# Optimization experiments

Measured on AMD Instinct MI355X. Metric: run time of the kernel, lower is better.

## Reference

```python
import jax, jax.numpy as jnp
import numpy as np

B, T, IN, H, K = 128, 4096, 2, 64, 2  # batch, seq_len, input feat, lstm hidden, num tags


def setup_inputs() -> dict:
    key = jax.random.key(0)
    ks = jax.random.split(key, 16)
    s = 1.0 / np.sqrt(H)
    u = lambda k, shape, a: jax.random.uniform(k, shape, jnp.float32, -a, a)
    p = {}
    p['x'] = jax.random.normal(ks[0], (B, T, IN), jnp.float32)
    # layer 0 (input IN), layer 1 (input 2H); leading dim 2 = [forward, backward] direction
    p['w_ih0'] = u(ks[1], (2, 4 * H, IN), s)
    p['w_hh0'] = u(ks[2], (2, 4 * H, H), s)
    p['b_ih0'] = u(ks[3], (2, 4 * H), s)
    p['b_hh0'] = u(ks[4], (2, 4 * H), s)
    p['w_ih1'] = u(ks[5], (2, 4 * H, 2 * H), s)
    p['w_hh1'] = u(ks[6], (2, 4 * H, H), s)
    p['b_ih1'] = u(ks[7], (2, 4 * H), s)
    p['b_hh1'] = u(ks[8], (2, 4 * H), s)
    p['fc_w'] = u(ks[9], (K, 2 * H), 1.0 / np.sqrt(2 * H))
    p['fc_b'] = u(ks[10], (K,), 1.0 / np.sqrt(2 * H))
    # CRF params (torchcrf init: U(-0.1, 0.1))
    p['trans'] = u(ks[11], (K, K), 0.1)
    p['start'] = u(ks[12], (K,), 0.1)
    p['end'] = u(ks[13], (K,), 0.1)
    return p


def _lstm_dir(xg, w_hh, b_hh):
    # xg: [T, B, 4H] precomputed input projections; PyTorch gate order i, f, g, o
    b, h = xg.shape[1], w_hh.shape[1]

    def step(carry, g_x):
        hs, cs = carry
        g = g_x + hs @ w_hh.T + b_hh
        i, f, gg, o = jnp.split(g, 4, axis=-1)
        cs = jax.nn.sigmoid(f) * cs + jax.nn.sigmoid(i) * jnp.tanh(gg)
        hs = jax.nn.sigmoid(o) * jnp.tanh(cs)
        return (hs, cs), hs

    init = (jnp.zeros((b, h), xg.dtype), jnp.zeros((b, h), xg.dtype))
    _, out = jax.lax.scan(step, init, xg)
    return out  # [T, B, H]


def _bilstm_layer(xt, w_ih, w_hh, b_ih, b_hh):
    # xt: [T, B, F] time-major input
    xg_f = jnp.einsum('tbi,gi->tbg', xt, w_ih[0]) + b_ih[0]
    xg_b = jnp.einsum('tbi,gi->tbg', xt[::-1], w_ih[1]) + b_ih[1]
    hf = _lstm_dir(xg_f, w_hh[0], b_hh[0])
    hb = _lstm_dir(xg_b, w_hh[1], b_hh[1])[::-1]
    return jnp.concatenate([hf, hb], axis=-1)  # [T, B, 2H]


def _viterbi(logits, trans, start, end):
    # logits: [B, T, K] -> best path [B, T]
    e = jnp.swapaxes(logits, 0, 1)  # [T, B, K]
    score0 = start[None, :] + e[0]

    def fwd(score, e_t):
        cand = score[:, :, None] + trans[None, :, :]  # [B, Kprev, Knext]
        bp = jnp.argmax(cand, axis=1)
        return jnp.max(cand, axis=1) + e_t, bp

    score, bps = jax.lax.scan(fwd, score0, e[1:])  # bps: [T-1, B, K]
    last = jnp.argmax(score + end[None, :], axis=-1)  # [B]

    def back(tag, bp):
        prev = jnp.take_along_axis(bp, tag[:, None], axis=1)[:, 0]
        return prev, prev

    _, path = jax.lax.scan(back, last, bps, reverse=True)  # [T-1, B]
    return jnp.swapaxes(jnp.concatenate([path, last[None, :]], axis=0), 0, 1)


def reference(x, w_ih0, w_hh0, b_ih0, b_hh0, w_ih1, w_hh1, b_ih1, b_hh1,
              fc_w, fc_b, trans, start, end):
    xt = jnp.swapaxes(x, 0, 1)  # [T, B, IN]
    h0 = _bilstm_layer(xt, w_ih0, w_hh0, b_ih0, b_hh0)
    h1 = _bilstm_layer(h0, w_ih1, w_hh1, b_ih1, b_hh1)  # [T, B, 2H]
    logits = jnp.swapaxes(jnp.einsum('tbh,kh->tbk', h1, fc_w) + fc_b, 0, 1)  # [B, T, K]
    return _viterbi(logits, trans, start, end).astype(jnp.int32)
```

## Files before the change

### kernel.cpp

```cpp
#include <hip/hip_runtime.h>

#define TT 4096
#define BATCH 128
#define HID 64
#define CK 32
#define NCH (TT / CK)
#define NSLOT (NCH + 1)

__device__ __forceinline__ float sigm(float x) { return 1.f / (1.f + expf(-x)); }
__device__ __forceinline__ float tanh_f(float x) { float e = expf(2.f * x); return 1.f - 2.f / (e + 1.f); }

__global__ __launch_bounds__(512, 2) void lstm_ckpt(
    const float* __restrict__ x,
    const float* __restrict__ w_ih,
    const float* __restrict__ w_hh,
    const float* __restrict__ b_ih, const float* __restrict__ b_hh,
    float* __restrict__ ckpt)
{
    const int blk = blockIdx.x;
    const int dir = blk & 1;
    const int b   = blk >> 1;
    const int tid = threadIdx.x;
    const int row = tid >> 1, half = tid & 1;

    __shared__ __align__(16) float xs[TT * 2];
    __shared__ __align__(16) float h_lds[HID];
    __shared__ __align__(16) float g_lds[256];

    {
        const float4* src = (const float4*)(x + (size_t)b * TT * 2);
        float4* dst = (float4*)xs;
        for (int rr = tid; rr < 2048; rr += 512) dst[rr] = src[rr];
    }
    const int grow = dir * 256 + row;
    float wv[32];
    {
        const float4* wr = (const float4*)(w_hh + (size_t)grow * 64) + half * 8;
        #pragma unroll
        for (int k = 0; k < 8; ++k) {
            float4 v = wr[k];
            wv[4*k] = v.x; wv[4*k+1] = v.y; wv[4*k+2] = v.z; wv[4*k+3] = v.w;
        }
    }
    const float wx0 = half ? 0.f : w_ih[grow * 2 + 0];
    const float wx1 = half ? 0.f : w_ih[grow * 2 + 1];
    const float bias = half ? 0.f : (b_ih[grow] + b_hh[grow]);
    const int gtype = row >> 6;
    float c = 0.f, hreg = 0.f;
    if (tid < HID) h_lds[tid] = 0.f;
    __syncthreads();

    for (int t = 0; t < TT; ++t) {
        const int tt = dir ? (TT - 1 - t) : t;
        if (tid < HID) {
            const int bnum = dir ? (tt + 1) : tt;
            if ((bnum & (CK - 1)) == 0) {
                float* cp = ckpt + (((size_t)(dir * BATCH + b) * NSLOT + (bnum >> 5)) << 7);
                cp[tid] = hreg; cp[HID + tid] = c;
            }
        }
        const float4* h4 = (const float4*)h_lds + half * 8;
        float a0 = 0.f, a1 = 0.f, a2 = 0.f, a3 = 0.f;
        #pragma unroll
        for (int k = 0; k < 8; ++k) {
            float4 hv = h4[k];
            a0 = fmaf(wv[4*k],   hv.x, a0);
            a1 = fmaf(wv[4*k+1], hv.y, a1);
            a2 = fmaf(wv[4*k+2], hv.z, a2);
            a3 = fmaf(wv[4*k+3], hv.w, a3);
        }
        float tot = (a0 + a1) + (a2 + a3);
        tot += __shfl_xor(tot, 1);
        if (half == 0) {
            const float acc = tot + bias + wx0 * xs[tt * 2] + wx1 * xs[tt * 2 + 1];
            g_lds[row] = (gtype == 2) ? tanh_f(acc) : sigm(acc);
        }
        __syncthreads();
        if (tid < HID) {
            const float iv = g_lds[tid], fv = g_lds[64 + tid], gg = g_lds[128 + tid], ov = g_lds[192 + tid];
            c = fv * c + iv * gg;
            hreg = ov * tanh_f(c);
            h_lds[tid] = hreg;
        }
        __syncthreads();
    }
}

__global__ __launch_bounds__(1024, 4) void lstm_fused1(
    const float* __restrict__ x,
    const float* __restrict__ w_ih0, const float* __restrict__ w_hh0,
    const float* __restrict__ b_ih0, const float* __restrict__ b_hh0,
    const float* __restrict__ w_ih1, const float* __restrict__ w_hh1,
    const float* __restrict__ b_ih1, const float* __restrict__ b_hh1,
    const float* __restrict__ fc_w,  const float* __restrict__ ckpt,
    float* __restrict__ plog)
{
    const int blk = blockIdx.x;
    const int l1dir = blk & 1;
    const int b = blk >> 1;
    const int tid = threadIdx.x;

    __shared__ __align__(16) float h0buf[2][CK][128];
    __shared__ __align__(16) float xg1[2][CK][256];
    __shared__ __align__(16) float xbuf[2][CK][2];
    __shared__ __align__(16) float g1[256];
    __shared__ __align__(16) float g0[2][256];
    __shared__ __align__(16) float h1b[2][HID];
    __shared__ __align__(16) float h0s[2][HID];

    const bool isL1 = tid < 256;
    const bool isL0 = (tid >= 256) && (tid < 768);
    const bool isG  = tid >= 768;
    const int q0 = tid - 256;
    const int d0 = (q0 >> 8) & 1;
    const int j0 = q0 & 255;
    const int jg = (tid - 768) & 255;

    float r[64];
    float bias_ = 0.f, wx0 = 0.f, wx1 = 0.f, fw0 = 0.f, fw1 = 0.f;
    float c1 = 0.f, c0 = 0.f, ckh = 0.f, ckc = 0.f;
    float4 xpre = make_float4(0.f, 0.f, 0.f, 0.f);
    float4 wc = make_float4(0.f, 0.f, 0.f, 0.f);
    const float4* wip4 = (const float4*)(w_ih1 + (size_t)(l1dir * 256 + jg) * 128);

    if (isL1) {
        const int grow = l1dir * 256 + tid;
        const float4* wr = (const float4*)(w_hh1 + (size_t)grow * 64);
        #pragma unroll
        for (int k = 0; k < 16; ++k) {
            float4 v = wr[k];
            r[4*k] = v.x; r[4*k+1] = v.y; r[4*k+2] = v.z; r[4*k+3] = v.w;
        }
        bias_ = b_ih1[grow] + b_hh1[grow];
        if (tid >= 64 && tid < 128) {
            fw0 = fc_w[l1dir * 64 + (tid - 64)];
            fw1 = fc_w[128 + l1dir * 64 + (tid - 64)];
        }
    } else if (isL0) {
        const int grow = d0 * 256 + j0;
        const float4* wr = (const float4*)(w_hh0 + (size_t)grow * 64);
        #pragma unroll
        for (int k = 0; k < 16; ++k) {
            float4 v = wr[k];
            r[4*k] = v.x; r[4*k+1] = v.y; r[4*k+2] = v.z; r[4*k+3] = v.w;
        }
        wx0 = w_ih0[grow * 2 + 0];
        wx1 = w_ih0[grow * 2 + 1];
        bias_ = b_ih0[grow] + b_hh0[grow];
    } else {
        #pragma unroll
        for (int k = 0; k < 32; ++k) r[k] = 0.f;
        wc = wip4[0];
    }

    if (tid < HID) { h1b[0][tid] = 0.f; h1b[1][tid] = 0.f; }
    {
        const int ac0 = l1dir ? (NCH - 1) : 0;
        if (tid < 16)
            ((float4*)xbuf[0])[tid] = ((const float4*)(x + ((size_t)b * TT + (size_t)ac0 * CK) * 2))[tid];
        if (isL0 && j0 < 64) {
            const int slot = d0 ? (ac0 + 1) : ac0;
            const float* cp = ckpt + (((size_t)(d0 * BATCH + b) * NSLOT + slot) << 7);
            h0s[d0][j0] = cp[j0];
            c0 = cp[HID + j0];
        }
    }
    __syncthreads();

    for (int i = -2; i < NCH; ++i) {
        const bool l1act = i >= 0;
        const bool gact  = (i + 1 >= 0) && (i + 1 < NCH);
        const bool l0act = (i + 2) < NCH;
        const int hbL0 = i & 1;
        const int hbG  = (i + 1) & 1;
        for (int s = 0; s < CK; ++s) {
            if (isG) {
                if (gact) {
                    float4 wn = wip4[(s + 1) & (CK - 1)];
                    const float4* hb = (const float4*)&h0buf[hbG][0][0] + s;
                    #pragma unroll
                    for (int s2 = 0; s2 < 32; ++s2) {
                        float4 hv = hb[s2 * 32];
                        float t0 = r[s2];
                        t0 = fmaf(wc.x, hv.x, t0);
                        t0 = fmaf(wc.y, hv.y, t0);
                        t0 = fmaf(wc.z, hv.z, t0);
                        t0 = fmaf(wc.w, hv.w, t0);
                        r[s2] = t0;
                    }
                    if (s == CK - 1) {
                        #pragma unroll
                        for (int s2 = 0; s2 < 32; ++s2) { xg1[hbG][s2][jg] = r[s2]; r[s2] = 0.f; }
                    }
                    wc = wn;
                }
            } else if (isL0) {
                if (s == 0 && j0 < 64 && (i + 3) < NCH) {
                    const int acn = l1dir ? (NCH - 1 - (i + 3)) : (i + 3);
                    const int slot = d0 ? (acn + 1) : acn;
                    const float* cp = ckpt + (((size_t)(d0 * BATCH + b) * NSLOT + slot) << 7);
                    ckh = cp[j0]; ckc = cp[HID + j0];
                }
                if (l0act) {
                    const int orow = d0 ? (CK - 1 - s) : s;
                    const float4* h4 = (const float4*)h0s[d0];
                    float a0 = 0.f, a1 = 0.f, a2 = 0.f, a3 = 0.f;
                    #pragma unroll
                    for (int k = 0; k < 16; ++k) {
                        float4 hv = h4[k];
                        a0 = fmaf(r[4*k],   hv.x, a0);
                        a1 = fmaf(r[4*k+1], hv.y, a1);
                        a2 = fmaf(r[4*k+2], hv.z, a2);
                        a3 = fmaf(r[4*k+3], hv.w, a3);
                    }
                    const float acc = bias_ + wx0 * xbuf[i & 1][orow][0] + wx1 * xbuf[i & 1][orow][1]
                                    + ((a0 + a1) + (a2 + a3));
                    g0[d0][j0] = ((j0 >> 6) == 2) ? tanh_f(acc) : sigm(acc);
                }
            } else {
                if (s == 0 && tid >= 128 && tid < 144 && (i + 3) < NCH) {
                    const int acn = l1dir ? (NCH - 1 - (i + 3)) : (i + 3);
                    xpre = ((const float4*)(x + ((size_t)b * TT + (size_t)acn * CK) * 2))[tid - 128];
                }
                if (l1act) {
                    const int u = i * CK + s;
                    const float4* h4 = (const float4*)h1b[u & 1];
                    float a0 = 0.f, a1 = 0.f, a2 = 0.f, a3 = 0.f;
                    #pragma unroll
                    for (int k = 0; k < 16; ++k) {
                        float4 hv = h4[k];
                        a0 = fmaf(r[4*k],   hv.x, a0);
                        a1 = fmaf(r[4*k+1], hv.y, a1);
                        a2 = fmaf(r[4*k+2], hv.z, a2);
                        a3 = fmaf(r[4*k+3], hv.w, a3);
                    }
                    const int srow = l1dir ? (CK - 1 - s) : s;
                    const float acc = bias_ + xg1[i & 1][srow][tid] + ((a0 + a1) + (a2 + a3));
                    g1[tid] = ((tid >> 6) == 2) ? tanh_f(acc) : sigm(acc);
                    if (tid >= 64 && tid < 128 && u > 0) {
                        const float hv = h1b[u & 1][tid - 64];
                        float p0 = hv * fw0, p1 = hv * fw1;
                        #pragma unroll
                        for (int d_ = 32; d_ > 0; d_ >>= 1) { p0 += __shfl_xor(p0, d_); p1 += __shfl_xor(p1, d_); }
                        if (tid == 64) {
                            const int tp = l1dir ? (TT - u) : (u - 1);
                            *(float2*)(plog + (((size_t)l1dir * BATCH + b) * TT + tp) * 2) = make_float2(p0, p1);
                        }
                    }
                }
            }
            __syncthreads();
            if (isL1) {
                if (l1act && tid < 64) {
                    const int u = i * CK + s;
                    const float iv = g1[tid], fv = g1[64 + tid], gg = g1[128 + tid], ov = g1[192 + tid];
                    c1 = fv * c1 + iv * gg;
                    h1b[(u + 1) & 1][tid] = ov * tanh_f(c1);
                }
                if (s == CK - 1 && tid >= 128 && tid < 144 && (i + 3) < NCH)
                    ((float4*)xbuf[(i + 1) & 1])[tid - 128] = xpre;
            } else if (isL0) {
                if (l0act && j0 < 64) {
                    const float iv = g0[d0][j0], fv = g0[d0][64 + j0], gg = g0[d0][128 + j0], ov = g0[d0][192 + j0];
                    c0 = fv * c0 + iv * gg;
                    const float hv = ov * tanh_f(c0);
                    const int orow = d0 ? (CK - 1 - s) : s;
                    h0buf[hbL0][orow][d0 * 64 + j0] = hv;
                    if (s == CK - 1 && (i + 3) < NCH) { h0s[d0][j0] = ckh; c0 = ckc; }
                    else h0s[d0][j0] = hv;
                }
            }
            __syncthreads();
        }
    }
    if (isL1 && tid >= 64 && tid < 128) {
        const float hv = h1b[0][tid - 64];
        float p0 = hv * fw0, p1 = hv * fw1;
        #pragma unroll
        for (int d_ = 32; d_ > 0; d_ >>= 1) { p0 += __shfl_xor(p0, d_); p1 += __shfl_xor(p1, d_); }
        if (tid == 64) {
            const int tp = l1dir ? 0 : (TT - 1);
            *(float2*)(plog + (((size_t)l1dir * BATCH + b) * TT + tp) * 2) = make_float2(p0, p1);
        }
    }
}

__device__ __forceinline__ unsigned long long shfl_u64(unsigned long long v, int src) {
    unsigned int lo = (unsigned int)v, hi = (unsigned int)(v >> 32);
    lo = __shfl(lo, src); hi = __shfl(hi, src);
    return ((unsigned long long)hi << 32) | lo;
}

__global__ __launch_bounds__(64, 1) void viterbi_k(
    const float* __restrict__ plog, const float* __restrict__ fc_b,
    const float* __restrict__ trans, const float* __restrict__ startv,
    const float* __restrict__ endv, int* __restrict__ out)
{
    const int b = blockIdx.x;
    const int lane = threadIdx.x;
    __shared__ __align__(16) float2 e_lds[64][65];

    const float fb0 = fc_b[0], fb1 = fc_b[1];
    const float* pf = plog + ((size_t)(0 * BATCH + b) * TT) * 2;
    const float* pb = plog + ((size_t)(1 * BATCH + b) * TT) * 2;
    for (int r = 0; r < 32; ++r) {
        const int i4 = r * 64 + lane;
        float4 a = ((const float4*)pf)[i4];
        float4 cc = ((const float4*)pb)[i4];
        const int t0 = 2 * i4, t1 = t0 + 1;
        e_lds[t0 & 63][t0 >> 6] = make_float2(a.x + cc.x + fb0, a.y + cc.y + fb1);
        e_lds[t1 & 63][t1 >> 6] = make_float2(a.z + cc.z + fb0, a.w + cc.w + fb1);
    }
    __syncthreads();
    const float tr00 = trans[0], tr01 = trans[1], tr10 = trans[2], tr11 = trans[3];
    const float2 e0 = e_lds[0][0];
    const float s00 = startv[0] + e0.x, s01 = startv[1] + e0.y;

    const int lo = lane * 64;
    const int hi = (lane == 63) ? (TT - 1) : (lo + 64);
    float a00, a01, a10, a11;
    {
        const float2 ee = e_lds[(lo + 1) & 63][(lo + 1) >> 6];
        a00 = tr00 + ee.x; a01 = tr01 + ee.y; a10 = tr10 + ee.x; a11 = tr11 + ee.y;
    }
    for (int t = lo + 2; t <= hi; ++t) {
        const float2 ee = e_lds[t & 63][t >> 6];
        const float n00 = fmaxf(a00 + tr00, a01 + tr10) + ee.x;
        const float n01 = fmaxf(a00 + tr01, a01 + tr11) + ee.y;
        const float n10 = fmaxf(a10 + tr00, a11 + tr10) + ee.x;
        const float n11 = fmaxf(a10 + tr01, a11 + tr11) + ee.y;
        a00 = n00; a01 = n01; a10 = n10; a11 = n11;
    }
    #pragma unroll
    for (int d = 1; d < 64; d <<= 1) {
        const float o00 = __shfl_up(a00, d), o01 = __shfl_up(a01, d);
        const float o10 = __shfl_up(a10, d), o11 = __shfl_up(a11, d);
        if (lane >= d) {
            const float n00 = fmaxf(o00 + a00, o01 + a10);
            const float n01 = fmaxf(o00 + a01, o01 + a11);
            const float n10 = fmaxf(o10 + a00, o11 + a10);
            const float n11 = fmaxf(o10 + a01, o11 + a11);
            a00 = n00; a01 = n01; a10 = n10; a11 = n11;
        }
    }
    const float p00 = __shfl_up(a00, 1), p01 = __shfl_up(a01, 1);
    const float p10 = __shfl_up(a10, 1), p11 = __shfl_up(a11, 1);
    float s0, s1;
    if (lane == 0) { s0 = s00; s1 = s01; }
    else { s0 = fmaxf(s00 + p00, s01 + p10); s1 = fmaxf(s00 + p01, s01 + p11); }
    unsigned long long m0 = 0ull, m1 = 0ull;
    for (int t = lo + 1; t <= hi; ++t) {
        const float2 ee = e_lds[t & 63][t >> 6];
        const float c00 = s0 + tr00, c10 = s1 + tr10;
        const float c01 = s0 + tr01, c11 = s1 + tr11;
        const int bp0 = c10 > c00, bp1 = c11 > c01;
        s0 = (bp0 ? c10 : c00) + ee.x;
        s1 = (bp1 ? c11 : c01) + ee.y;
        m0 |= (unsigned long long)bp0 << (t - lo - 1);
        m1 |= (unsigned long long)bp1 << (t - lo - 1);
    }
    int last;
    {
        const int lt = (s1 + endv[1]) > (s0 + endv[0]);
        last = __shfl(lt, 63);
    }
    int f0 = 0, f1 = 1;
    for (int t = hi; t > lo; --t) {
        const int s_ = t - lo - 1;
        f0 = (int)(((f0 ? m1 : m0) >> s_) & 1ull);
        f1 = (int)(((f1 ? m1 : m0) >> s_) & 1ull);
    }
    int mm = f0 | (f1 << 1);
    #pragma unroll
    for (int d = 1; d < 64; d <<= 1) {
        const int mo = __shfl_down(mm, d);
        if (lane + d < 64) {
            const int r0 = (mm >> (mo & 1)) & 1;
            const int r1 = (mm >> ((mo >> 1) & 1)) & 1;
            mm = r0 | (r1 << 1);
        }
    }
    const int gn = __shfl_down(mm, 1);
    int cur = (lane == 63) ? last : ((gn >> last) & 1);
    unsigned long long tagm = 0ull;
    if (lane == 63) tagm |= (unsigned long long)last << 63;
    for (int t = hi; t > lo; --t) {
        const int s_ = t - lo - 1;
        cur = (int)(((cur ? m1 : m0) >> s_) & 1ull);
        tagm |= (unsigned long long)cur << s_;
    }
    int* ob = out + (size_t)b * TT;
    for (int r = 0; r < 64; ++r) {
        const unsigned long long mr = shfl_u64(tagm, r);
        ob[r * 64 + lane] = (int)((mr >> lane) & 1ull);
    }
}

extern "C" void kernel_launch(void* const* d_in, const int* in_sizes, int n_in,
                              void* d_out, int out_size, void* d_ws, size_t ws_size,
                              hipStream_t stream) {
    const float* x      = (const float*)d_in[0];
    const float* w_ih0  = (const float*)d_in[1];
    const float* w_hh0  = (const float*)d_in[2];
    const float* b_ih0  = (const float*)d_in[3];
    const float* b_hh0  = (const float*)d_in[4];
    const float* w_ih1  = (const float*)d_in[5];
    const float* w_hh1  = (const float*)d_in[6];
    const float* b_ih1  = (const float*)d_in[7];
    const float* b_hh1  = (const float*)d_in[8];
    const float* fc_w   = (const float*)d_in[9];
    const float* fc_b   = (const float*)d_in[10];
    const float* trans  = (const float*)d_in[11];
    const float* startv = (const float*)d_in[12];
    const float* endv   = (const float*)d_in[13];

    char* ws = (char*)d_ws;
    const size_t ckpt_bytes = (size_t)2 * BATCH * NSLOT * 128 * 4;
    float* ckpt = (float*)ws;
    float* plog = (float*)(ws + ckpt_bytes);

    lstm_ckpt<<<256, 512, 0, stream>>>(x, w_ih0, w_hh0, b_ih0, b_hh0, ckpt);
    lstm_fused1<<<256, 1024, 0, stream>>>(x, w_ih0, w_hh0, b_ih0, b_hh0,
                                          w_ih1, w_hh1, b_ih1, b_hh1,
                                          fc_w, ckpt, plog);
    viterbi_k<<<128, 64, 0, stream>>>(plog, fc_b, trans, startv, endv, (int*)d_out);
}
```

Before: 8.248 ms.

## Merge fused LSTM roles into 256 threads each doing L1, L0 and projection work

```diff
diff --git a/kernel.cpp b/kernel.cpp
--- a/kernel.cpp
+++ b/kernel.cpp
@@ -86,7 +86,7 @@
     }
 }
 
-__global__ __launch_bounds__(1024, 4) void lstm_fused1(
+__global__ __launch_bounds__(256, 1) void lstm_fused1(
     const float* __restrict__ x,
     const float* __restrict__ w_ih0, const float* __restrict__ w_hh0,
     const float* __restrict__ b_ih0, const float* __restrict__ b_hh0,
@@ -108,49 +108,56 @@
     __shared__ __align__(16) float h1b[2][HID];
     __shared__ __align__(16) float h0s[2][HID];
 
-    const bool isL1 = tid < 256;
-    const bool isL0 = (tid >= 256) && (tid < 768);
-    const bool isG  = tid >= 768;
-    const int q0 = tid - 256;
-    const int d0 = (q0 >> 8) & 1;
-    const int j0 = q0 & 255;
-    const int jg = (tid - 768) & 255;
-
-    float r[64];
-    float bias_ = 0.f, wx0 = 0.f, wx1 = 0.f, fw0 = 0.f, fw1 = 0.f;
+    const int dg = tid >> 7;
+    const int j  = tid & 127;
+    const int du = tid >> 6;
+    const int eu = tid & 63;
+
+    float wl1[64];
+    float wl0[128];
+    float acc[32];
+    float4 wc;
+    float biasL1, biasA, biasB, wxA0, wxA1, wxB0, wxB1;
+    float fw0 = 0.f, fw1 = 0.f;
     float c1 = 0.f, c0 = 0.f, ckh = 0.f, ckc = 0.f;
-    float4 xpre = make_float4(0.f, 0.f, 0.f, 0.f);
-    float4 wc = make_float4(0.f, 0.f, 0.f, 0.f);
-    const float4* wip4 = (const float4*)(w_ih1 + (size_t)(l1dir * 256 + jg) * 128);
-
-    if (isL1) {
+    const float4* wip4 = (const float4*)(w_ih1 + (size_t)(l1dir * 256 + tid) * 128);
+
+    {
         const int grow = l1dir * 256 + tid;
         const float4* wr = (const float4*)(w_hh1 + (size_t)grow * 64);
         #pragma unroll
         for (int k = 0; k < 16; ++k) {
             float4 v = wr[k];
-            r[4*k] = v.x; r[4*k+1] = v.y; r[4*k+2] = v.z; r[4*k+3] = v.w;
-        }
-        bias_ = b_ih1[grow] + b_hh1[grow];
-        if (tid >= 64 && tid < 128) {
-            fw0 = fc_w[l1dir * 64 + (tid - 64)];
-            fw1 = fc_w[128 + l1dir * 64 + (tid - 64)];
-        }
-    } else if (isL0) {
-        const int grow = d0 * 256 + j0;
-        const float4* wr = (const float4*)(w_hh0 + (size_t)grow * 64);
+            wl1[4*k] = v.x; wl1[4*k+1] = v.y; wl1[4*k+2] = v.z; wl1[4*k+3] = v.w;
+        }
+        biasL1 = b_ih1[grow] + b_hh1[grow];
+    }
+    {
+        const int rA = dg * 256 + j;
+        const int rB = rA + 128;
+        const float4* wa = (const float4*)(w_hh0 + (size_t)rA * 64);
+        const float4* wb = (const float4*)(w_hh0 + (size_t)rB * 64);
         #pragma unroll
         for (int k = 0; k < 16; ++k) {
-            float4 v = wr[k];
-            r[4*k] = v.x; r[4*k+1] = v.y; r[4*k+2] = v.z; r[4*k+3] = v.w;
-        }
-        wx0 = w_ih0[grow * 2 + 0];
-        wx1 = w_ih0[grow * 2 + 1];
-        bias_ = b_ih0[grow] + b_hh0[grow];
-    } else {
-        #pragma unroll
-        for (int k = 0; k < 32; ++k) r[k] = 0.f;
-        wc = wip4[0];
+            float4 v = wa[k];
+            wl0[4*k] = v.x; wl0[4*k+1] = v.y; wl0[4*k+2] = v.z; wl0[4*k+3] = v.w;
+        }
+        #pragma unroll
+        for (int k = 0; k < 16; ++k) {
+            float4 v = wb[k];
+            wl0[64+4*k] = v.x; wl0[64+4*k+1] = v.y; wl0[64+4*k+2] = v.z; wl0[64+4*k+3] = v.w;
+        }
+        wxA0 = w_ih0[rA * 2 + 0]; wxA1 = w_ih0[rA * 2 + 1];
+        wxB0 = w_ih0[rB * 2 + 0]; wxB1 = w_ih0[rB * 2 + 1];
+        biasA = b_ih0[rA] + b_hh0[rA];
+        biasB = b_ih0[rB] + b_hh0[rB];
+    }
+    #pragma unroll
+    for (int k = 0; k < 32; ++k) acc[k] = 0.f;
+    wc = wip4[0];
+    if (tid >= 128 && tid < 192) {
+        fw0 = fc_w[l1dir * 64 + (tid - 128)];
+        fw1 = fc_w[128 + l1dir * 64 + (tid - 128)];
     }
 
     if (tid < HID) { h1b[0][tid] = 0.f; h1b[1][tid] = 0.f; }
@@ -158,11 +165,11 @@
         const int ac0 = l1dir ? (NCH - 1) : 0;
         if (tid < 16)
             ((float4*)xbuf[0])[tid] = ((const float4*)(x + ((size_t)b * TT + (size_t)ac0 * CK) * 2))[tid];
-        if (isL0 && j0 < 64) {
-            const int slot = d0 ? (ac0 + 1) : ac0;
-            const float* cp = ckpt + (((size_t)(d0 * BATCH + b) * NSLOT + slot) << 7);
-            h0s[d0][j0] = cp[j0];
-            c0 = cp[HID + j0];
+        if (tid < 128) {
+            const int slot = du ? (ac0 + 1) : ac0;
+            const float* cp = ckpt + (((size_t)(du * BATCH + b) * NSLOT + slot) << 7);
+            h0s[du][eu] = cp[eu];
+            c0 = cp[HID + eu];
         }
     }
     __syncthreads();
@@ -174,111 +181,110 @@
         const int hbL0 = i & 1;
         const int hbG  = (i + 1) & 1;
         for (int s = 0; s < CK; ++s) {
-            if (isG) {
-                if (gact) {
-                    float4 wn = wip4[(s + 1) & (CK - 1)];
-                    const float4* hb = (const float4*)&h0buf[hbG][0][0] + s;
+            if (s == 0 && (i + 3) < NCH) {
+                const int acn = l1dir ? (NCH - 1 - (i + 3)) : (i + 3);
+                if (tid < 128) {
+                    const int slot = du ? (acn + 1) : acn;
+                    const float* cp = ckpt + (((size_t)(du * BATCH + b) * NSLOT + slot) << 7);
+                    ckh = cp[eu]; ckc = cp[HID + eu];
+                }
+                if (tid >= 192 && tid < 208)
+                    ((float4*)xbuf[(i + 1) & 1])[tid - 192] =
+                        ((const float4*)(x + ((size_t)b * TT + (size_t)acn * CK) * 2))[tid - 192];
+            }
+            if (gact) {
+                float4 wn = wip4[(s + 1) & (CK - 1)];
+                const float4* hb = (const float4*)&h0buf[hbG][0][0] + s;
+                #pragma unroll
+                for (int s2 = 0; s2 < 32; ++s2) {
+                    float4 hv = hb[s2 * 32];
+                    float t0 = acc[s2];
+                    t0 = fmaf(wc.x, hv.x, t0);
+                    t0 = fmaf(wc.y, hv.y, t0);
+                    t0 = fmaf(wc.z, hv.z, t0);
+                    t0 = fmaf(wc.w, hv.w, t0);
+                    acc[s2] = t0;
+                }
+                if (s == CK - 1) {
                     #pragma unroll
-                    for (int s2 = 0; s2 < 32; ++s2) {
-                        float4 hv = hb[s2 * 32];
-                        float t0 = r[s2];
-                        t0 = fmaf(wc.x, hv.x, t0);
-                        t0 = fmaf(wc.y, hv.y, t0);
-                        t0 = fmaf(wc.z, hv.z, t0);
-                        t0 = fmaf(wc.w, hv.w, t0);
-                        r[s2] = t0;
+                    for (int s2 = 0; s2 < 32; ++s2) { xg1[hbG][s2][tid] = acc[s2]; acc[s2] = 0.f; }
+                }
+                wc = wn;
+            }
+            if (l0act) {
+                const int orow = dg ? (CK - 1 - s) : s;
+                const float4* h4 = (const float4*)h0s[dg];
+                float a0 = 0.f, a1 = 0.f, a2 = 0.f, a3 = 0.f;
+                float e0 = 0.f, e1 = 0.f, e2 = 0.f, e3 = 0.f;
+                #pragma unroll
+                for (int k = 0; k < 16; ++k) {
+                    float4 hv = h4[k];
+                    a0 = fmaf(wl0[4*k],   hv.x, a0);
+                    a1 = fmaf(wl0[4*k+1], hv.y, a1);
+                    a2 = fmaf(wl0[4*k+2], hv.z, a2);
+                    a3 = fmaf(wl0[4*k+3], hv.w, a3);
+                    e0 = fmaf(wl0[64+4*k],   hv.x, e0);
+                    e1 = fmaf(wl0[64+4*k+1], hv.y, e1);
+                    e2 = fmaf(wl0[64+4*k+2], hv.z, e2);
+                    e3 = fmaf(wl0[64+4*k+3], hv.w, e3);
+                }
+                const float xv0 = xbuf[i & 1][orow][0], xv1 = xbuf[i & 1][orow][1];
+                const float accA = biasA + ((a0 + a1) + (a2 + a3)) + wxA0 * xv0 + wxA1 * xv1;
+                const float accB = biasB + ((e0 + e1) + (e2 + e3)) + wxB0 * xv0 + wxB1 * xv1;
+                g0[dg][j]       = sigm(accA);
+                g0[dg][j + 128] = (j < 64) ? tanh_f(accB) : sigm(accB);
+            }
+            if (l1act) {
+                const int u = i * CK + s;
+                const float4* h14 = (const float4*)h1b[u & 1];
+                float a0 = 0.f, a1 = 0.f, a2 = 0.f, a3 = 0.f;
+                #pragma unroll
+                for (int k = 0; k < 16; ++k) {
+                    float4 hv = h14[k];
+                    a0 = fmaf(wl1[4*k],   hv.x, a0);
+                    a1 = fmaf(wl1[4*k+1], hv.y, a1);
+                    a2 = fmaf(wl1[4*k+2], hv.z, a2);
+                    a3 = fmaf(wl1[4*k+3], hv.w, a3);
+                }
+                const int srow = l1dir ? (CK - 1 - s) : s;
+                const float accL = biasL1 + xg1[i & 1][srow][tid] + ((a0 + a1) + (a2 + a3));
+                g1[tid] = ((tid >> 6) == 2) ? tanh_f(accL) : sigm(accL);
+                if (tid >= 128 && tid < 192 && u > 0) {
+                    const float hv = h1b[u & 1][tid - 128];
+                    float p0 = hv * fw0, p1 = hv * fw1;
+                    #pragma unroll
+                    for (int d_ = 32; d_ > 0; d_ >>= 1) { p0 += __shfl_xor(p0, d_); p1 += __shfl_xor(p1, d_); }
+                    if (tid == 128) {
+                        const int tp = l1dir ? (TT - u) : (u - 1);
+                        *(float2*)(plog + (((size_t)l1dir * BATCH + b) * TT + tp) * 2) = make_float2(p0, p1);
                     }
-                    if (s == CK - 1) {
-                        #pragma unroll
-                        for (int s2 = 0; s2 < 32; ++s2) { xg1[hbG][s2][jg] = r[s2]; r[s2] = 0.f; }
-                    }
-                    wc = wn;
-                }
-            } else if (isL0) {
-                if (s == 0 && j0 < 64 && (i + 3) < NCH) {
-                    const int acn = l1dir ? (NCH - 1 - (i + 3)) : (i + 3);
-                    const int slot = d0 ? (acn + 1) : acn;
-                    const float* cp = ckpt + (((size_t)(d0 * BATCH + b) * NSLOT + slot) << 7);
-                    ckh = cp[j0]; ckc = cp[HID + j0];
-                }
-                if (l0act) {
-                    const int orow = d0 ? (CK - 1 - s) : s;
-                    const float4* h4 = (const float4*)h0s[d0];
-                    float a0 = 0.f, a1 = 0.f, a2 = 0.f, a3 = 0.f;
-                    #pragma unroll
-                    for (int k = 0; k < 16; ++k) {
-                        float4 hv = h4[k];
-                        a0 = fmaf(r[4*k],   hv.x, a0);
-                        a1 = fmaf(r[4*k+1], hv.y, a1);
-                        a2 = fmaf(r[4*k+2], hv.z, a2);
-                        a3 = fmaf(r[4*k+3], hv.w, a3);
-                    }
-                    const float acc = bias_ + wx0 * xbuf[i & 1][orow][0] + wx1 * xbuf[i & 1][orow][1]
-                                    + ((a0 + a1) + (a2 + a3));
-                    g0[d0][j0] = ((j0 >> 6) == 2) ? tanh_f(acc) : sigm(acc);
-                }
-            } else {
-                if (s == 0 && tid >= 128 && tid < 144 && (i + 3) < NCH) {
-                    const int acn = l1dir ? (NCH - 1 - (i + 3)) : (i + 3);
-                    xpre = ((const float4*)(x + ((size_t)b * TT + (size_t)acn * CK) * 2))[tid - 128];
-                }
-                if (l1act) {
-                    const int u = i * CK + s;
-                    const float4* h4 = (const float4*)h1b[u & 1];
-                    float a0 = 0.f, a1 = 0.f, a2 = 0.f, a3 = 0.f;
-                    #pragma unroll
-                    for (int k = 0; k < 16; ++k) {
-                        float4 hv = h4[k];
-                        a0 = fmaf(r[4*k],   hv.x, a0);
-                        a1 = fmaf(r[4*k+1], hv.y, a1);
-                        a2 = fmaf(r[4*k+2], hv.z, a2);
-                        a3 = fmaf(r[4*k+3], hv.w, a3);
-                    }
-                    const int srow = l1dir ? (CK - 1 - s) : s;
-                    const float acc = bias_ + xg1[i & 1][srow][tid] + ((a0 + a1) + (a2 + a3));
-                    g1[tid] = ((tid >> 6) == 2) ? tanh_f(acc) : sigm(acc);
-                    if (tid >= 64 && tid < 128 && u > 0) {
-                        const float hv = h1b[u & 1][tid - 64];
-                        float p0 = hv * fw0, p1 = hv * fw1;
-                        #pragma unroll
-                        for (int d_ = 32; d_ > 0; d_ >>= 1) { p0 += __shfl_xor(p0, d_); p1 += __shfl_xor(p1, d_); }
-                        if (tid == 64) {
-                            const int tp = l1dir ? (TT - u) : (u - 1);
-                            *(float2*)(plog + (((size_t)l1dir * BATCH + b) * TT + tp) * 2) = make_float2(p0, p1);
-                        }
-                    }
                 }
             }
             __syncthreads();
-            if (isL1) {
-                if (l1act && tid < 64) {
-                    const int u = i * CK + s;
-                    const float iv = g1[tid], fv = g1[64 + tid], gg = g1[128 + tid], ov = g1[192 + tid];
-                    c1 = fv * c1 + iv * gg;
-                    h1b[(u + 1) & 1][tid] = ov * tanh_f(c1);
-                }
-                if (s == CK - 1 && tid >= 128 && tid < 144 && (i + 3) < NCH)
-                    ((float4*)xbuf[(i + 1) & 1])[tid - 128] = xpre;
-            } else if (isL0) {
-                if (l0act && j0 < 64) {
-                    const float iv = g0[d0][j0], fv = g0[d0][64 + j0], gg = g0[d0][128 + j0], ov = g0[d0][192 + j0];
-                    c0 = fv * c0 + iv * gg;
-                    const float hv = ov * tanh_f(c0);
-                    const int orow = d0 ? (CK - 1 - s) : s;
-                    h0buf[hbL0][orow][d0 * 64 + j0] = hv;
-                    if (s == CK - 1 && (i + 3) < NCH) { h0s[d0][j0] = ckh; c0 = ckc; }
-                    else h0s[d0][j0] = hv;
-                }
+            if (l1act && tid < 64) {
+                const int u = i * CK + s;
+                const float iv = g1[tid], fv = g1[64 + tid], gg = g1[128 + tid], ov = g1[192 + tid];
+                c1 = fv * c1 + iv * gg;
+                h1b[(u + 1) & 1][tid] = ov * tanh_f(c1);
+            }
+            if (l0act && tid < 128) {
+                const float iv = g0[du][eu], fv = g0[du][64 + eu], gg = g0[du][128 + eu], ov = g0[du][192 + eu];
+                c0 = fv * c0 + iv * gg;
+                const float hv = ov * tanh_f(c0);
+                const int orow = du ? (CK - 1 - s) : s;
+                h0buf[hbL0][orow][du * 64 + eu] = hv;
+                if (s == CK - 1 && (i + 3) < NCH) { h0s[du][eu] = ckh; c0 = ckc; }
+                else h0s[du][eu] = hv;
             }
             __syncthreads();
         }
     }
-    if (isL1 && tid >= 64 && tid < 128) {
-        const float hv = h1b[0][tid - 64];
+    if (tid >= 128 && tid < 192) {
+        const float hv = h1b[0][tid - 128];
         float p0 = hv * fw0, p1 = hv * fw1;
         #pragma unroll
         for (int d_ = 32; d_ > 0; d_ >>= 1) { p0 += __shfl_xor(p0, d_); p1 += __shfl_xor(p1, d_); }
-        if (tid == 64) {
+        if (tid == 128) {
             const int tp = l1dir ? 0 : (TT - 1);
             *(float2*)(plog + (((size_t)l1dir * BATCH + b) * TT + tp) * 2) = make_float2(p0, p1);
         }
@@ -420,8 +426,8 @@
     float* plog = (float*)(ws + ckpt_bytes);
 
     lstm_ckpt<<<256, 512, 0, stream>>>(x, w_ih0, w_hh0, b_ih0, b_hh0, ckpt);
-    lstm_fused1<<<256, 1024, 0, stream>>>(x, w_ih0, w_hh0, b_ih0, b_hh0,
-                                          w_ih1, w_hh1, b_ih1, b_hh1,
-                                          fc_w, ckpt, plog);
+    lstm_fused1<<<256, 256, 0, stream>>>(x, w_ih0, w_hh0, b_ih0, b_hh0,
+                                         w_ih1, w_hh1, b_ih1, b_hh1,
+                                         fc_w, ckpt, plog);
     viterbi_k<<<128, 64, 0, stream>>>(plog, fc_b, trans, startv, endv, (int*)d_out);
 }
```

Measured after the change: 14.22 ms. 1.72x slower.
